# Kernel optimization log

Hardware: AMD Instinct MI355X
Metric: run time of the kernel (lower is better)

## Reference

```python
import jax, jax.numpy as jnp
import numpy as np

B, LR_DIM, G_DIM, K, D, T = 256, 1024, 512, 64, 256, 8
GRID = jnp.linspace(-4.0, 4.0, 41)  # registered buffer in torch module


def _mu_bell(x, c, a_bell, b_bell):
    # generalized bell membership, clamp(a,b) >= 1e-3 as in torch
    a = jnp.maximum(a_bell, 1e-3)
    b = jnp.maximum(b_bell, 1e-3)
    return 1.0 / (1.0 + jnp.abs((x - c) / a) ** (2.0 * b))


def _mu_s(x, a, b):
    eps = 1e-12
    a2 = jnp.minimum(a, b)
    b2 = jnp.maximum(a, b)
    mid = (a2 + b2) * 0.5
    up = 2.0 * ((x - a2) / (b2 - a2 + eps)) ** 2
    dn = 1.0 - 2.0 * ((b2 - x) / (b2 - a2 + eps)) ** 2
    y = jnp.where((x > a2) & (x <= mid), up, jnp.zeros_like(x))
    y = jnp.where((x > mid) & (x <= b2), dn, y)
    return jnp.where(x > b2, jnp.ones_like(x), y)


def _fuzzify(x, a_bell, b_bell):
    # x: (B,d) -> (B,2d)
    xs = 4.0 * jnp.tanh(x / 4.0)
    xb = _mu_bell(xs, 0.0, a_bell, b_bell)
    xS = _mu_s(xs, -1.0, 1.0)
    return jnp.concatenate([xb, xS], axis=-1)


def _defuzzify(rt, a_bell, b_bell):
    # rt: (B,2d) -> centroid (B,d)
    d = rt.shape[1] // 2
    rb, rs = rt[:, :d], rt[:, d:]
    g = GRID[None, None, :]                      # (1,1,G)
    c_b = 4.0 * jnp.tanh(rb)[..., None]          # (B,d,1)
    c_s = 4.0 * jnp.tanh(rs)[..., None]
    mu_b = _mu_bell(g, c_b, a_bell, b_bell)      # (B,d,G)
    a_s = jnp.clip(c_s - 1.0, -4.0, 4.0)
    b_s = jnp.clip(c_s + 1.0, -4.0, 4.0)
    mu_s = _mu_s(g, a_s, b_s)
    cen_b = (g * mu_b).sum(-1) / (mu_b.sum(-1) + 1e-12)
    cen_s = (g * mu_s).sum(-1) / (mu_s.sum(-1) + 1e-12)
    return 0.5 * cen_b + 0.5 * cen_s


def _forward(wsi_lr, genomics, FT, W_lr, b_lr, W_g, b_g, WqI, WqG, WkI, WkG,
             WvI, WvG, mlp_W1, mlp_b1, mlp_W2, mlp_b2, Wf, bf, Wi, bi, Vf, Vi,
             a_bell, b_bell):
    scale = jnp.float32(D) ** 0.5
    lr = wsi_lr @ W_lr + b_lr                    # (B,d)
    g = genomics @ W_g + b_g
    lr_f = _fuzzify(lr, a_bell, b_bell)          # (B,2d)
    g_f = _fuzzify(g, a_bell, b_bell)
    QI = lr_f @ WqI                              # (B,d), loop-invariant
    QG = g_f @ WqG
    Ft0 = jnp.broadcast_to(FT[None], (wsi_lr.shape[0],) + FT.shape)  # (B,K,d)

    def step(Ft, _):
        sI = jnp.einsum('bd,bkd->bk', QI, Ft @ WkI) / scale
        sG = jnp.einsum('bd,bkd->bk', QG, Ft @ WkG) / scale
        rtI = jnp.einsum('bk,bke->be', jax.nn.softmax(sI, axis=-1), Ft @ WvI)  # (B,2d)
        rtG = jnp.einsum('bk,bke->be', jax.nn.softmax(sG, axis=-1), Ft @ WvG)
        r = 0.5 * _defuzzify(rtI, a_bell, b_bell) + 0.5 * _defuzzify(rtG, a_bell, b_bell)
        rb = jnp.broadcast_to(r[:, None, :], Ft.shape)              # (B,K,d)
        x = Ft + rb
        F_tilde = jax.nn.gelu(x @ mlp_W1 + mlp_b1, approximate=False) @ mlp_W2 + mlp_b2 + x
        f_gate = jax.nn.sigmoid(rb @ Wf + bf + jnp.tanh(Ft @ Vf))
        i_gate = jax.nn.sigmoid(rb @ Wi + bi + jnp.tanh(Ft @ Vi))
        Ft_new = f_gate * Ft + i_gate * jnp.tanh(F_tilde)
        return Ft_new, Ft_new

    _, steps = jax.lax.scan(step, Ft0, None, length=T)
    # torch stores step `T-s` result at index s-1: list index 0 holds the LAST
    # computed state, index T-1 the first -> reverse chronological order
    return steps[::-1]  # (T,B,K,d)


def setup_inputs() -> dict:
    key = jax.random.key(0)
    ks = jax.random.split(key, 20)

    def rn(k, shape, scale):
        return jax.random.normal(k, shape, dtype=jnp.float32) * scale

    z = lambda *s: jnp.zeros(s, jnp.float32)
    return dict(
        wsi_lr=rn(ks[0], (B, LR_DIM), 1.0),
        genomics=rn(ks[1], (B, G_DIM), 1.0),
        FT=rn(ks[2], (K, D), 0.02),
        W_lr=rn(ks[3], (LR_DIM, D), LR_DIM ** -0.5), b_lr=z(D),
        W_g=rn(ks[4], (G_DIM, D), G_DIM ** -0.5), b_g=z(D),
        WqI=rn(ks[5], (2 * D, D), (2 * D) ** -0.5),
        WqG=rn(ks[6], (2 * D, D), (2 * D) ** -0.5),
        WkI=rn(ks[7], (D, D), D ** -0.5),
        WkG=rn(ks[8], (D, D), D ** -0.5),
        WvI=rn(ks[9], (D, 2 * D), D ** -0.5),
        WvG=rn(ks[10], (D, 2 * D), D ** -0.5),
        mlp_W1=rn(ks[11], (D, 2 * D), D ** -0.5), mlp_b1=z(2 * D),
        mlp_W2=rn(ks[12], (2 * D, D), (2 * D) ** -0.5), mlp_b2=z(D),
        Wf=rn(ks[13], (D, D), D ** -0.5), bf=z(D),
        Wi=rn(ks[14], (D, D), D ** -0.5), bi=z(D),
        Vf=rn(ks[15], (D, D), D ** -0.5),
        Vi=rn(ks[16], (D, D), D ** -0.5),
        a_bell=jnp.float32(1.0),
        b_bell=jnp.float32(2.0),
    )


def reference(wsi_lr, genomics, FT, W_lr, b_lr, W_g, b_g, WqI, WqG, WkI, WkG,
              WvI, WvG, mlp_W1, mlp_b1, mlp_W2, mlp_b2, Wf, bf, Wi, bi, Vf, Vi,
              a_bell, b_bell):
    return _forward(wsi_lr, genomics, FT, W_lr, b_lr, W_g, b_g, WqI, WqG, WkI,
                    WkG, WvI, WvG, mlp_W1, mlp_b1, mlp_W2, mlp_b2, Wf, bf, Wi,
                    bi, Vf, Vi, a_bell, b_bell)
```

## Files before the change

### kernel.cpp

```cpp
#include <hip/hip_runtime.h>
#include <hip/hip_bf16.h>

#define B_    256
#define K_    64
#define D_    256
#define T_    8
#define NROW  (B_*K_)

typedef short short8v __attribute__((ext_vector_type(8)));
typedef float f32x4  __attribute__((ext_vector_type(4)));

__device__ __forceinline__ float fexp2(float x) { return __builtin_amdgcn_exp2f(x); }
__device__ __forceinline__ float flog2(float x) { return __builtin_amdgcn_logf(x); }

__device__ __forceinline__ float sigmoid_f(float x) {
  return 1.f / (1.f + fexp2(x * -1.4426950408889634f));
}
__device__ __forceinline__ float tanh_fast(float x) {
  float xc = fminf(fmaxf(x, -30.f), 30.f);
  float t = fexp2(xc * 2.8853900817779268f);
  return (t - 1.f) / (t + 1.f);
}
__device__ __forceinline__ float gelu_f(float x) {
  return 0.5f * x * (1.f + erff(x * 0.70710678118654752440f));
}
__device__ __forceinline__ unsigned short f2bf(float x) {
  __hip_bfloat16 h = __float2bfloat16(x);
  return *reinterpret_cast<unsigned short*>(&h);
}
__device__ __forceinline__ float bfss(unsigned short s) {
  return __uint_as_float(((unsigned int)s) << 16);
}
__device__ __forceinline__ float muS_f(float x, float a2, float b2) {
  float mid = 0.5f * (a2 + b2);
  float inv = 1.f / (b2 - a2 + 1e-12f);
  if (x > b2)  return 1.f;
  if (x > mid) { float u = (b2 - x) * inv; return 1.f - 2.f * u * u; }
  if (x > a2)  { float u = (x - a2) * inv; return 2.f * u * u; }
  return 0.f;
}
__device__ __forceinline__ float pow_abs(float z, float e2b) {
  return fexp2(e2b * flog2(fabsf(z)));
}
__device__ __forceinline__ float defuzz_one(float rb_, float rs_, float ab, float bb) {
  float e2b = 2.f * bb;
  float inv_ab = 1.f / ab;
  float cb = 4.f * tanh_fast(rb_);
  float num = 0.f, den = 0.f;
  #pragma unroll
  for (int j = 0; j < 41; ++j) {
    float gj = -4.f + 0.2f * (float)j;
    float mu = 1.f / (1.f + pow_abs((gj - cb) * inv_ab, e2b));
    num += gj * mu; den += mu;
  }
  float cenb = num / (den + 1e-12f);
  float cs = 4.f * tanh_fast(rs_);
  float as_ = fminf(fmaxf(cs - 1.f, -4.f), 4.f);
  float bs_ = fminf(fmaxf(cs + 1.f, -4.f), 4.f);
  num = 0.f; den = 0.f;
  {
    float mid = 0.5f * (as_ + bs_);
    float inv = 1.f / (bs_ - as_ + 1e-12f);
    #pragma unroll
    for (int j = 0; j < 41; ++j) {
      float gj = -4.f + 0.2f * (float)j;
      float mu;
      if (gj > bs_)      mu = 1.f;
      else if (gj > mid) { float u = (bs_ - gj) * inv; mu = 1.f - 2.f * u * u; }
      else if (gj > as_) { float u = (gj - as_) * inv; mu = 2.f * u * u; }
      else               mu = 0.f;
      num += gj * mu; den += mu;
    }
  }
  float cens = num / (den + 1e-12f);
  return 0.5f * cenb + 0.5f * cens;
}

__global__ __launch_bounds__(256) void k_convert(
    const float* __restrict__ W1, const float* __restrict__ Vf, const float* __restrict__ Vi,
    const float* __restrict__ W2, const float* __restrict__ FT,
    const float* __restrict__ WkI, const float* __restrict__ WkG,
    const float* __restrict__ WvI, const float* __restrict__ WvG,
    const float* __restrict__ Wf,  const float* __restrict__ Wi,
    unsigned short* __restrict__ B1t, unsigned short* __restrict__ W2t,
    unsigned short* __restrict__ FTbf,
    float* __restrict__ WkIt, float* __restrict__ WkGt,
    unsigned short* __restrict__ Wv2, unsigned short* __restrict__ WB)
{
  int idx = blockIdx.x * 256 + threadIdx.x;
  if (idx < 262144) {
    int n = idx >> 8, k = idx & 255;
    float v = (n < 512) ? W1[(size_t)k*512 + n]
            : (n < 768) ? Vf[(size_t)k*256 + (n-512)]
                        : Vi[(size_t)k*256 + (n-768)];
    B1t[idx] = f2bf(v);
  } else if (idx < 393216) {
    int j = idx - 262144;
    int n = j >> 9, k = j & 511;
    W2t[j] = f2bf(W2[(size_t)k*256 + n]);
  } else if (idx < 409600) {
    int j = idx - 393216;
    FTbf[j] = f2bf(FT[j]);
  } else if (idx < 475136) {
    int j = idx - 409600;
    int k = j >> 8, n = j & 255;
    WkIt[j] = WkI[(size_t)n*256 + k];
  } else if (idx < 540672) {
    int j = idx - 475136;
    int k = j >> 8, n = j & 255;
    WkGt[j] = WkG[(size_t)n*256 + k];
  } else if (idx < 802816) {
    int j = idx - 540672;
    int d = j >> 10, c = j & 1023;
    float v = (c < 512) ? WvI[(size_t)d*512 + c] : WvG[(size_t)d*512 + (c-512)];
    Wv2[j] = f2bf(v);
  } else if (idx < 1064960) {
    int j = idx - 802816;
    int d = j >> 10, c = j & 1023;
    float v = (c < 512) ? W1[(size_t)d*512 + c]
            : (c < 768) ? Wf[(size_t)d*256 + (c-512)]
                        : Wi[(size_t)d*256 + (c-768)];
    WB[j] = f2bf(v);
  }
}

__global__ __launch_bounds__(256) void k_pre_lin(
    const float* __restrict__ wsi, const float* __restrict__ gen,
    const float* __restrict__ W_lr, const float* __restrict__ b_lr,
    const float* __restrict__ W_g,  const float* __restrict__ b_g,
    const float* __restrict__ a_p,  const float* __restrict__ b_p,
    float* __restrict__ lrf, float* __restrict__ gf)
{
  int g_ix = blockIdx.x;
  int half = g_ix >> 4, tile = g_ix & 15;
  int bx = tile & 3, by = tile >> 2;
  int n0 = bx * 64, m0 = by * 64;
  const float* A    = half ? gen  : wsi;
  const float* Bm   = half ? W_g  : W_lr;
  const float* bias = half ? b_g  : b_lr;
  float* outp       = half ? gf   : lrf;
  int KK            = half ? 512  : 1024;
  float ab = fmaxf(a_p[0], 0.001f), bb = fmaxf(b_p[0], 0.001f);
  float e2b = 2.f * bb, inv_ab = 1.f / ab;

  __shared__ float As[16][64];
  __shared__ float Bs[16][64];
  int tid = threadIdx.x, tx = tid & 15, ty = tid >> 4;
  float acc[4][4] = {};
  int am = tid >> 2, ak = (tid & 3) * 4;
  int bk = tid >> 4, bn = (tid & 15) * 4;
  const float* arow = A + (size_t)(m0 + am) * KK;
  for (int k0 = 0; k0 < KK; k0 += 16) {
    float4 av = *(const float4*)(arow + k0 + ak);
    As[ak+0][am] = av.x; As[ak+1][am] = av.y; As[ak+2][am] = av.z; As[ak+3][am] = av.w;
    *(float4*)&Bs[bk][bn] = *(const float4*)(Bm + (size_t)(k0 + bk) * 256 + n0 + bn);
    __syncthreads();
    #pragma unroll
    for (int kk = 0; kk < 16; ++kk) {
      float a0 = As[kk][ty*4+0], a1 = As[kk][ty*4+1], a2 = As[kk][ty*4+2], a3 = As[kk][ty*4+3];
      float b0 = Bs[kk][tx*4+0], b1 = Bs[kk][tx*4+1], b2 = Bs[kk][tx*4+2], b3 = Bs[kk][tx*4+3];
      acc[0][0]=fmaf(a0,b0,acc[0][0]); acc[0][1]=fmaf(a0,b1,acc[0][1]); acc[0][2]=fmaf(a0,b2,acc[0][2]); acc[0][3]=fmaf(a0,b3,acc[0][3]);
      acc[1][0]=fmaf(a1,b0,acc[1][0]); acc[1][1]=fmaf(a1,b1,acc[1][1]); acc[1][2]=fmaf(a1,b2,acc[1][2]); acc[1][3]=fmaf(a1,b3,acc[1][3]);
      acc[2][0]=fmaf(a2,b0,acc[2][0]); acc[2][1]=fmaf(a2,b1,acc[2][1]); acc[2][2]=fmaf(a2,b2,acc[2][2]); acc[2][3]=fmaf(a2,b3,acc[2][3]);
      acc[3][0]=fmaf(a3,b0,acc[3][0]); acc[3][1]=fmaf(a3,b1,acc[3][1]); acc[3][2]=fmaf(a3,b2,acc[3][2]); acc[3][3]=fmaf(a3,b3,acc[3][3]);
    }
    __syncthreads();
  }
  #pragma unroll
  for (int i = 0; i < 4; ++i) {
    int row = m0 + ty*4 + i;
    #pragma unroll
    for (int j = 0; j < 4; ++j) {
      int col = n0 + tx*4 + j;
      float v = acc[i][j] + bias[col];
      float xs = 4.f * tanh_fast(v * 0.25f);
      outp[(size_t)row*512 + col]       = 1.f / (1.f + pow_abs(xs * inv_ab, e2b));
      outp[(size_t)row*512 + col + 256] = muS_f(xs, -1.f, 1.f);
    }
  }
}

__global__ __launch_bounds__(256) void k_pre_q(
    const float* __restrict__ lrf, const float* __restrict__ gf,
    const float* __restrict__ WqI, const float* __restrict__ WqG,
    float* __restrict__ QI, float* __restrict__ QG)
{
  int g_ix = blockIdx.x;
  int half = g_ix >> 4, tile = g_ix & 15;
  int bx = tile & 3, by = tile >> 2;
  int n0 = bx * 64, m0 = by * 64;
  const float* A  = half ? gf  : lrf;
  const float* Bm = half ? WqG : WqI;
  float* outp     = half ? QG  : QI;

  __shared__ float As[16][64];
  __shared__ float Bs[16][64];
  int tid = threadIdx.x, tx = tid & 15, ty = tid >> 4;
  float acc[4][4] = {};
  int am = tid >> 2, ak = (tid & 3) * 4;
  int bk = tid >> 4, bn = (tid & 15) * 4;
  const float* arow = A + (size_t)(m0 + am) * 512;
  for (int k0 = 0; k0 < 512; k0 += 16) {
    float4 av = *(const float4*)(arow + k0 + ak);
    As[ak+0][am] = av.x; As[ak+1][am] = av.y; As[ak+2][am] = av.z; As[ak+3][am] = av.w;
    *(float4*)&Bs[bk][bn] = *(const float4*)(Bm + (size_t)(k0 + bk) * 256 + n0 + bn);
    __syncthreads();
    #pragma unroll
    for (int kk = 0; kk < 16; ++kk) {
      float a0 = As[kk][ty*4+0], a1 = As[kk][ty*4+1], a2 = As[kk][ty*4+2], a3 = As[kk][ty*4+3];
      float b0 = Bs[kk][tx*4+0], b1 = Bs[kk][tx*4+1], b2 = Bs[kk][tx*4+2], b3 = Bs[kk][tx*4+3];
      acc[0][0]=fmaf(a0,b0,acc[0][0]); acc[0][1]=fmaf(a0,b1,acc[0][1]); acc[0][2]=fmaf(a0,b2,acc[0][2]); acc[0][3]=fmaf(a0,b3,acc[0][3]);
      acc[1][0]=fmaf(a1,b0,acc[1][0]); acc[1][1]=fmaf(a1,b1,acc[1][1]); acc[1][2]=fmaf(a1,b2,acc[1][2]); acc[1][3]=fmaf(a1,b3,acc[1][3]);
      acc[2][0]=fmaf(a2,b0,acc[2][0]); acc[2][1]=fmaf(a2,b1,acc[2][1]); acc[2][2]=fmaf(a2,b2,acc[2][2]); acc[2][3]=fmaf(a2,b3,acc[2][3]);
      acc[3][0]=fmaf(a3,b0,acc[3][0]); acc[3][1]=fmaf(a3,b1,acc[3][1]); acc[3][2]=fmaf(a3,b2,acc[3][2]); acc[3][3]=fmaf(a3,b3,acc[3][3]);
    }
    __syncthreads();
  }
  #pragma unroll
  for (int i = 0; i < 4; ++i) {
    float4 v = make_float4(acc[i][0], acc[i][1], acc[i][2], acc[i][3]);
    *(float4*)(outp + (size_t)(m0 + ty*4 + i) * 256 + n0 + tx*4) = v;
  }
}

__global__ __launch_bounds__(256) void k_pre_qp(
    const float* __restrict__ QI, const float* __restrict__ QG,
    const float* __restrict__ WkIt, const float* __restrict__ WkGt,
    float* __restrict__ qIp, float* __restrict__ qGp)
{
  int g_ix = blockIdx.x;
  int half = g_ix >> 4, tile = g_ix & 15;
  int bx = tile & 3, by = tile >> 2;
  int n0 = bx * 64, m0 = by * 64;
  const float* A  = half ? QG   : QI;
  const float* Bm = half ? WkGt : WkIt;
  float* outp     = half ? qGp  : qIp;

  __shared__ float As[16][64];
  __shared__ float Bs[16][64];
  int tid = threadIdx.x, tx = tid & 15, ty = tid >> 4;
  float acc[4][4] = {};
  int am = tid >> 2, ak = (tid & 3) * 4;
  int bk = tid >> 4, bn = (tid & 15) * 4;
  const float* arow = A + (size_t)(m0 + am) * 256;
  for (int k0 = 0; k0 < 256; k0 += 16) {
    float4 av = *(const float4*)(arow + k0 + ak);
    As[ak+0][am] = av.x; As[ak+1][am] = av.y; As[ak+2][am] = av.z; As[ak+3][am] = av.w;
    *(float4*)&Bs[bk][bn] = *(const float4*)(Bm + (size_t)(k0 + bk) * 256 + n0 + bn);
    __syncthreads();
    #pragma unroll
    for (int kk = 0; kk < 16; ++kk) {
      float a0 = As[kk][ty*4+0], a1 = As[kk][ty*4+1], a2 = As[kk][ty*4+2], a3 = As[kk][ty*4+3];
      float b0 = Bs[kk][tx*4+0], b1 = Bs[kk][tx*4+1], b2 = Bs[kk][tx*4+2], b3 = Bs[kk][tx*4+3];
      acc[0][0]=fmaf(a0,b0,acc[0][0]); acc[0][1]=fmaf(a0,b1,acc[0][1]); acc[0][2]=fmaf(a0,b2,acc[0][2]); acc[0][3]=fmaf(a0,b3,acc[0][3]);
      acc[1][0]=fmaf(a1,b0,acc[1][0]); acc[1][1]=fmaf(a1,b1,acc[1][1]); acc[1][2]=fmaf(a1,b2,acc[1][2]); acc[1][3]=fmaf(a1,b3,acc[1][3]);
      acc[2][0]=fmaf(a2,b0,acc[2][0]); acc[2][1]=fmaf(a2,b1,acc[2][1]); acc[2][2]=fmaf(a2,b2,acc[2][2]); acc[2][3]=fmaf(a2,b3,acc[2][3]);
      acc[3][0]=fmaf(a3,b0,acc[3][0]); acc[3][1]=fmaf(a3,b1,acc[3][1]); acc[3][2]=fmaf(a3,b2,acc[3][2]); acc[3][3]=fmaf(a3,b3,acc[3][3]);
    }
    __syncthreads();
  }
  #pragma unroll
  for (int i = 0; i < 4; ++i) {
    float4 v = make_float4(acc[i][0], acc[i][1], acc[i][2], acc[i][3]);
    *(float4*)(outp + (size_t)(m0 + ty*4 + i) * 256 + n0 + tx*4) = v;
  }
}

__global__ __launch_bounds__(512) void k_scan(
    const unsigned short* __restrict__ FTbf, const float* __restrict__ FTf,
    const float* __restrict__ qIp, const float* __restrict__ qGp,
    const unsigned short* __restrict__ Wv2, const unsigned short* __restrict__ WB,
    const float* __restrict__ b1, const float* __restrict__ bfv,
    const float* __restrict__ biv, const float* __restrict__ b2,
    const unsigned short* __restrict__ B1t, const unsigned short* __restrict__ W2t,
    const float* __restrict__ a_p, const float* __restrict__ b_p,
    unsigned short* __restrict__ Gf, unsigned short* __restrict__ Gi,
    float* __restrict__ out)
{
  __shared__ __align__(16) short Fs[64*264];
  __shared__ __align__(16) short Bstage[64*264];
  __shared__ __align__(16) short Wstage[256*72];
  __shared__ __align__(16) short A2ch[64*72];
  __shared__ float qv[512];
  __shared__ float red[512];
  __shared__ float prl[128];
  __shared__ float ftb[512];
  __shared__ float rL[256];
  __shared__ float rWall[1024];

  int b = blockIdx.x, tid = threadIdx.x;
  int w = tid >> 6, lane = tid & 63, lr = lane & 15, lh = lane >> 4;
  int rg = w & 3, cg = w >> 2;
  float ab = fmaxf(a_p[0], 0.001f), bb = fmaxf(b_p[0], 0.001f);

  #pragma unroll
  for (int p = 0; p < 4; ++p) {
    int idx = (p*512 + tid) * 8;
    int row = idx >> 8, col = idx & 255;
    *(float4*)&Fs[row*264 + col] = *(const float4*)&FTbf[idx];
  }
  qv[tid] = (tid < 256) ? qIp[(size_t)b*256 + tid] : qGp[(size_t)b*256 + tid - 256];
  __syncthreads();

  const float* Fprev = nullptr;
  for (int st = 0; st < T_; ++st) {
    float* Fout = out + (size_t)(7 - st) * NROW * 256;

    {
      int which = tid >> 8, tt = tid & 255, k = tt & 63, part = tt >> 6;
      const unsigned int* frow = (const unsigned int*)&Fs[k*264 + part*64];
      const float* q0 = qv + which*256 + part*64;
      float s0 = 0.f;
      #pragma unroll
      for (int d2 = 0; d2 < 32; ++d2) {
        unsigned int pr = frow[d2];
        float f0 = __uint_as_float(pr << 16);
        float f1 = __uint_as_float(pr & 0xffff0000u);
        s0 = fmaf(f1, q0[2*d2+1], fmaf(f0, q0[2*d2], s0));
      }
      red[which*256 + tt] = s0;
    }
    __syncthreads();
    if (tid < 128) {
      int which = tid >> 6, kk = tid & 63;
      const float* rp = red + which*256;
      float s = (rp[kk] + rp[64+kk] + rp[128+kk] + rp[192+kk]) * (1.f/16.f);
      float m = s;
      for (int off = 32; off; off >>= 1) m = fmaxf(m, __shfl_xor(m, off, 64));
      float e = fexp2((s - m) * 1.4426950408889634f);
      float sum = e;
      for (int off = 32; off; off >>= 1) sum += __shfl_xor(sum, off, 64);
      prl[which*64 + kk] = e / sum;
    }
    __syncthreads();
    {
      int which = tid >> 8, tt = tid & 255;
      const float* pp = prl + which*64;
      float f0 = 0.f;
      #pragma unroll 8
      for (int kk = 0; kk < 64; ++kk)
        f0 = fmaf(pp[kk], bfss((unsigned short)Fs[kk*264 + tt]), f0);
      ftb[which*256 + tt] = f0;
    }
    __syncthreads();
    {
      int half = tid >> 8, tt = tid & 255;
      const float* fb = ftb + half*256;
      const unsigned short* wv = Wv2 + half*512 + tt;
      float a0 = 0.f, a1 = 0.f;
      #pragma unroll 4
      for (int d = 0; d < 256; ++d) {
        float fv = fb[d];
        a0 = fmaf(fv, bfss(wv[(size_t)d*1024]),       a0);
        a1 = fmaf(fv, bfss(wv[(size_t)d*1024 + 256]), a1);
      }
      red[half*256 + tt] = defuzz_one(a0, a1, ab, bb);
    }
    __syncthreads();
    if (tid < 256) rL[tid] = 0.5f * (red[tid] + red[256 + tid]);
    __syncthreads();
    {
      float w0 = 0.f, w1 = 0.f;
      const unsigned short* wb0 = WB + tid;
      #pragma unroll 4
      for (int d = 0; d < 256; ++d) {
        float rv = rL[d];
        w0 = fmaf(rv, bfss(wb0[(size_t)d*1024]),       w0);
        w1 = fmaf(rv, bfss(wb0[(size_t)d*1024 + 512]), w1);
      }
      rWall[tid]       = w0 + b1[tid];
      int tt = tid & 255;
      rWall[512 + tid] = w1 + ((tid < 256) ? bfv[tt] : biv[tt]);
    }
    __syncthreads();

    for (int c = 8; c < 16; ++c) {
      #pragma unroll
      for (int p = 0; p < 4; ++p) {
        int idx = (p*512 + tid) * 8;
        int row = idx >> 8, col = idx & 255;
        *(float4*)&Bstage[row*264 + col] = *(const float4*)&B1t[(size_t)c*16384 + idx];
      }
      __syncthreads();
      #pragma unroll
      for (int f = 0; f < 2; ++f) {
        f32x4 acc = {0.f,0.f,0.f,0.f};
        int nb = cg*32 + f*16;
        #pragma unroll
        for (int ks = 0; ks < 8; ++ks) {
          short8v av = *(const short8v*)&Fs[(rg*16 + lr)*264 + ks*32 + lh*8];
          short8v bv = *(const short8v*)&Bstage[(nb + lr)*264 + ks*32 + lh*8];
          acc = __builtin_amdgcn_mfma_f32_16x16x32_bf16(av, bv, acc, 0, 0, 0);
        }
        int gc = c*64 + nb + lr;
        float add = rWall[gc];
        int cc = gc - 512;
        #pragma unroll
        for (int r = 0; r < 4; ++r) {
          int row = b*64 + rg*16 + lh*4 + r;
          unsigned short val = f2bf(sigmoid_f(add + tanh_fast(acc[r])));
          if (cc < 256) Gf[(size_t)row*256 + cc]       = val;
          else          Gi[(size_t)row*256 + cc - 256] = val;
        }
      }
      __syncthreads();
    }

    f32x4 O[8];
    #pragma unroll
    for (int nn = 0; nn < 8; ++nn) { O[nn][0]=0.f; O[nn][1]=0.f; O[nn][2]=0.f; O[nn][3]=0.f; }
    for (int c = 0; c < 8; ++c) {
      #pragma unroll
      for (int p = 0; p < 4; ++p) {
        int idx = (p*512 + tid) * 8;
        int row = idx >> 8, col = idx & 255;
        *(float4*)&Bstage[row*264 + col] = *(const float4*)&B1t[(size_t)c*16384 + idx];
      }
      #pragma unroll
      for (int p = 0; p < 4; ++p) {
        int idx = (p*512 + tid) * 8;
        int n = idx >> 6, kk = idx & 63;
        *(float4*)&Wstage[n*72 + kk] = *(const float4*)&W2t[(size_t)n*512 + c*64 + kk];
      }
      __syncthreads();
      #pragma unroll
      for (int f = 0; f < 2; ++f) {
        f32x4 acc = {0.f,0.f,0.f,0.f};
        int nb = cg*32 + f*16;
        #pragma unroll
        for (int ks = 0; ks < 8; ++ks) {
          short8v av = *(const short8v*)&Fs[(rg*16 + lr)*264 + ks*32 + lh*8];
          short8v bv = *(const short8v*)&Bstage[(nb + lr)*264 + ks*32 + lh*8];
          acc = __builtin_amdgcn_mfma_f32_16x16x32_bf16(av, bv, acc, 0, 0, 0);
        }
        int gc = c*64 + nb + lr;
        float add = rWall[gc];
        #pragma unroll
        for (int r = 0; r < 4; ++r)
          A2ch[(rg*16 + lh*4 + r)*72 + nb + lr] = f2bf(gelu_f(acc[r] + add));
      }
      __syncthreads();
      #pragma unroll
      for (int ks2 = 0; ks2 < 2; ++ks2) {
        short8v av = *(const short8v*)&A2ch[(rg*16 + lr)*72 + ks2*32 + lh*8];
        #pragma unroll
        for (int nn = 0; nn < 8; ++nn) {
          short8v bv = *(const short8v*)&Wstage[(cg*128 + nn*16 + lr)*72 + ks2*32 + lh*8];
          O[nn] = __builtin_amdgcn_mfma_f32_16x16x32_bf16(av, bv, O[nn], 0, 0, 0);
        }
      }
      __syncthreads();
    }

    #pragma unroll
    for (int nn = 0; nn < 8; ++nn) {
      int col = cg*128 + nn*16 + lr;
      float b2c = b2[col], rv = rL[col];
      #pragma unroll
      for (int r = 0; r < 4; ++r) {
        int rowl = rg*16 + lh*4 + r;
        int row = b*64 + rowl;
        float Ftv = (st == 0) ? FTf[rowl*256 + col] : Fprev[(size_t)row*256 + col];
        float ftld = O[nn][r] + b2c + Ftv + rv;
        float fg = bfss(Gf[(size_t)row*256 + col]);
        float ig = bfss(Gi[(size_t)row*256 + col]);
        float ov = fg * Ftv + ig * tanh_fast(ftld);
        Fout[(size_t)row*256 + col] = ov;
        Fs[rowl*264 + col] = f2bf(ov);
      }
    }
    Fprev = Fout;
    __syncthreads();
  }
}

extern "C" void kernel_launch(void* const* d_in, const int* in_sizes, int n_in,
                              void* d_out, int out_size, void* d_ws, size_t ws_size,
                              hipStream_t stream)
{
  (void)in_sizes; (void)n_in; (void)out_size; (void)ws_size;
  const float* wsi  = (const float*)d_in[0];
  const float* gen  = (const float*)d_in[1];
  const float* FT   = (const float*)d_in[2];
  const float* W_lr = (const float*)d_in[3];
  const float* b_lr = (const float*)d_in[4];
  const float* W_g  = (const float*)d_in[5];
  const float* b_g  = (const float*)d_in[6];
  const float* WqI  = (const float*)d_in[7];
  const float* WqG  = (const float*)d_in[8];
  const float* WkI  = (const float*)d_in[9];
  const float* WkG  = (const float*)d_in[10];
  const float* WvI  = (const float*)d_in[11];
  const float* WvG  = (const float*)d_in[12];
  const float* W1   = (const float*)d_in[13];
  const float* b1   = (const float*)d_in[14];
  const float* W2   = (const float*)d_in[15];
  const float* b2   = (const float*)d_in[16];
  const float* Wf   = (const float*)d_in[17];
  const float* bf   = (const float*)d_in[18];
  const float* Wi   = (const float*)d_in[19];
  const float* bi   = (const float*)d_in[20];
  const float* Vf   = (const float*)d_in[21];
  const float* Vi   = (const float*)d_in[22];
  const float* a_p  = (const float*)d_in[23];
  const float* b_p  = (const float*)d_in[24];

  float* out = (float*)d_out;
  float* ws  = (float*)d_ws;
  float* qIp   = ws;
  float* qGp   = qIp   + 65536;
  float* lrf   = qGp   + 65536;
  float* gf    = lrf   + 131072;
  float* QI    = gf    + 131072;
  float* QG    = QI    + 65536;
  float* WkIt  = QG    + 65536;
  float* WkGt  = WkIt  + 65536;
  unsigned short* Gfb  = (unsigned short*)(WkGt + 65536);
  unsigned short* Gib  = Gfb  + 4194304;
  unsigned short* FTbf = Gib  + 4194304;
  unsigned short* B1t  = FTbf + 16384;
  unsigned short* W2t  = B1t  + 262144;
  unsigned short* Wv2  = W2t  + 131072;
  unsigned short* WB   = Wv2  + 262144;

  k_convert<<<4160, 256, 0, stream>>>(W1, Vf, Vi, W2, FT, WkI, WkG, WvI, WvG, Wf, Wi,
                                      B1t, W2t, FTbf, WkIt, WkGt, Wv2, WB);
  k_pre_lin<<<32, 256, 0, stream>>>(wsi, gen, W_lr, b_lr, W_g, b_g, a_p, b_p, lrf, gf);
  k_pre_q<<<32, 256, 0, stream>>>(lrf, gf, WqI, WqG, QI, QG);
  k_pre_qp<<<32, 256, 0, stream>>>(QI, QG, WkIt, WkGt, qIp, qGp);

  k_scan<<<256, 512, 0, stream>>>(FTbf, FT, qIp, qGp, Wv2, WB,
                                  b1, bf, bi, b2, B1t, W2t, a_p, b_p,
                                  Gfb, Gib, out);
}
```

Before: 871.7 us.

## Pre-pack MFMA weight fragments and read B operands directly from global memory

```diff
diff --git a/kernel.cpp b/kernel.cpp
--- a/kernel.cpp
+++ b/kernel.cpp
@@ -82,22 +82,25 @@
     const float* __restrict__ WkI, const float* __restrict__ WkG,
     const float* __restrict__ WvI, const float* __restrict__ WvG,
     const float* __restrict__ Wf,  const float* __restrict__ Wi,
-    unsigned short* __restrict__ B1t, unsigned short* __restrict__ W2t,
+    unsigned short* __restrict__ B1p, unsigned short* __restrict__ W2p,
     unsigned short* __restrict__ FTbf,
     float* __restrict__ WkIt, float* __restrict__ WkGt,
     unsigned short* __restrict__ Wv2, unsigned short* __restrict__ WB)
 {
   int idx = blockIdx.x * 256 + threadIdx.x;
   if (idx < 262144) {
-    int n = idx >> 8, k = idx & 255;
+    int q = idx;
+    int c = q >> 14, ks = (q >> 11) & 7, row = (q >> 5) & 63, j = q & 31;
+    int n = c*64 + row, k = ks*32 + j;
     float v = (n < 512) ? W1[(size_t)k*512 + n]
             : (n < 768) ? Vf[(size_t)k*256 + (n-512)]
                         : Vi[(size_t)k*256 + (n-768)];
-    B1t[idx] = f2bf(v);
+    B1p[idx] = f2bf(v);
   } else if (idx < 393216) {
-    int j = idx - 262144;
-    int n = j >> 9, k = j & 511;
-    W2t[j] = f2bf(W2[(size_t)k*256 + n]);
+    int q = idx - 262144;
+    int c = q >> 14, ks2 = (q >> 13) & 1, n = (q >> 5) & 255, j = q & 31;
+    int k = c*64 + ks2*32 + j;
+    W2p[q] = f2bf(W2[(size_t)k*256 + n]);
   } else if (idx < 409600) {
     int j = idx - 393216;
     FTbf[j] = f2bf(FT[j]);
@@ -272,14 +275,12 @@
     const unsigned short* __restrict__ Wv2, const unsigned short* __restrict__ WB,
     const float* __restrict__ b1, const float* __restrict__ bfv,
     const float* __restrict__ biv, const float* __restrict__ b2,
-    const unsigned short* __restrict__ B1t, const unsigned short* __restrict__ W2t,
+    const unsigned short* __restrict__ B1p, const unsigned short* __restrict__ W2p,
     const float* __restrict__ a_p, const float* __restrict__ b_p,
     unsigned short* __restrict__ Gf, unsigned short* __restrict__ Gi,
     float* __restrict__ out)
 {
   __shared__ __align__(16) short Fs[64*264];
-  __shared__ __align__(16) short Bstage[64*264];
-  __shared__ __align__(16) short Wstage[256*72];
   __shared__ __align__(16) short A2ch[64*72];
   __shared__ float qv[512];
   __shared__ float red[512];
@@ -376,20 +377,13 @@
 
     for (int c = 8; c < 16; ++c) {
       #pragma unroll
-      for (int p = 0; p < 4; ++p) {
-        int idx = (p*512 + tid) * 8;
-        int row = idx >> 8, col = idx & 255;
-        *(float4*)&Bstage[row*264 + col] = *(const float4*)&B1t[(size_t)c*16384 + idx];
-      }
-      __syncthreads();
-      #pragma unroll
       for (int f = 0; f < 2; ++f) {
         f32x4 acc = {0.f,0.f,0.f,0.f};
         int nb = cg*32 + f*16;
         #pragma unroll
         for (int ks = 0; ks < 8; ++ks) {
           short8v av = *(const short8v*)&Fs[(rg*16 + lr)*264 + ks*32 + lh*8];
-          short8v bv = *(const short8v*)&Bstage[(nb + lr)*264 + ks*32 + lh*8];
+          short8v bv = *(const short8v*)&B1p[(size_t)((c*8 + ks)*64 + nb + lr)*32 + lh*8];
           acc = __builtin_amdgcn_mfma_f32_16x16x32_bf16(av, bv, acc, 0, 0, 0);
         }
         int gc = c*64 + nb + lr;
@@ -403,26 +397,12 @@
           else          Gi[(size_t)row*256 + cc - 256] = val;
         }
       }
-      __syncthreads();
     }
 
     f32x4 O[8];
     #pragma unroll
     for (int nn = 0; nn < 8; ++nn) { O[nn][0]=0.f; O[nn][1]=0.f; O[nn][2]=0.f; O[nn][3]=0.f; }
     for (int c = 0; c < 8; ++c) {
-      #pragma unroll
-      for (int p = 0; p < 4; ++p) {
-        int idx = (p*512 + tid) * 8;
-        int row = idx >> 8, col = idx & 255;
-        *(float4*)&Bstage[row*264 + col] = *(const float4*)&B1t[(size_t)c*16384 + idx];
-      }
-      #pragma unroll
-      for (int p = 0; p < 4; ++p) {
-        int idx = (p*512 + tid) * 8;
-        int n = idx >> 6, kk = idx & 63;
-        *(float4*)&Wstage[n*72 + kk] = *(const float4*)&W2t[(size_t)n*512 + c*64 + kk];
-      }
-      __syncthreads();
       #pragma unroll
       for (int f = 0; f < 2; ++f) {
         f32x4 acc = {0.f,0.f,0.f,0.f};
@@ -430,7 +410,7 @@
         #pragma unroll
         for (int ks = 0; ks < 8; ++ks) {
           short8v av = *(const short8v*)&Fs[(rg*16 + lr)*264 + ks*32 + lh*8];
-          short8v bv = *(const short8v*)&Bstage[(nb + lr)*264 + ks*32 + lh*8];
+          short8v bv = *(const short8v*)&B1p[(size_t)((c*8 + ks)*64 + nb + lr)*32 + lh*8];
           acc = __builtin_amdgcn_mfma_f32_16x16x32_bf16(av, bv, acc, 0, 0, 0);
         }
         int gc = c*64 + nb + lr;
@@ -445,8 +425,8 @@
         short8v av = *(const short8v*)&A2ch[(rg*16 + lr)*72 + ks2*32 + lh*8];
         #pragma unroll
         for (int nn = 0; nn < 8; ++nn) {
-          short8v bv = *(const short8v*)&Wstage[(cg*128 + nn*16 + lr)*72 + ks2*32 + lh*8];
-          O[nn] = __builtin_amdgcn_mfma_f32_16x16x32_bf16(av, bv, O[nn], 0, 0, 0);
+          short8v bw = *(const short8v*)&W2p[(size_t)((c*2 + ks2)*256 + cg*128 + nn*16 + lr)*32 + lh*8];
+          O[nn] = __builtin_amdgcn_mfma_f32_16x16x32_bf16(av, bw, O[nn], 0, 0, 0);
         }
       }
       __syncthreads();
@@ -518,18 +498,18 @@
   unsigned short* Gfb  = (unsigned short*)(WkGt + 65536);
   unsigned short* Gib  = Gfb  + 4194304;
   unsigned short* FTbf = Gib  + 4194304;
-  unsigned short* B1t  = FTbf + 16384;
-  unsigned short* W2t  = B1t  + 262144;
-  unsigned short* Wv2  = W2t  + 131072;
+  unsigned short* B1p  = FTbf + 16384;
+  unsigned short* W2p  = B1p  + 262144;
+  unsigned short* Wv2  = W2p  + 131072;
   unsigned short* WB   = Wv2  + 262144;
 
   k_convert<<<4160, 256, 0, stream>>>(W1, Vf, Vi, W2, FT, WkI, WkG, WvI, WvG, Wf, Wi,
-                                      B1t, W2t, FTbf, WkIt, WkGt, Wv2, WB);
+                                      B1p, W2p, FTbf, WkIt, WkGt, Wv2, WB);
   k_pre_lin<<<32, 256, 0, stream>>>(wsi, gen, W_lr, b_lr, W_g, b_g, a_p, b_p, lrf, gf);
   k_pre_q<<<32, 256, 0, stream>>>(lrf, gf, WqI, WqG, QI, QG);
   k_pre_qp<<<32, 256, 0, stream>>>(QI, QG, WkIt, WkGt, qIp, qGp);
 
   k_scan<<<256, 512, 0, stream>>>(FTbf, FT, qIp, qGp, Wv2, WB,
-                                  b1, bf, bi, b2, B1t, W2t, a_p, b_p,
+                                  b1, bf, bi, b2, B1p, W2p, a_p, b_p,
                                   Gfb, Gib, out);
 }
```

New measurement: 1.492 ms. +71.1%, slower.
